# Kernel tuning notes

Measured on AMD Instinct MI355X. Metric: run time of the kernel, lower is better.

The kernel has to match this reference:

```python
import jax, jax.numpy as jnp
import numpy as np

K = 16
D = 1024
B = 65536

# Row-major off-diagonal index order matching the torch double loop (i, j, i != j)
_ii, _jj = np.nonzero(~np.eye(K, dtype=bool))  # each (K*(K-1),), row-major
OFF_I = jnp.asarray(_ii)
OFF_J = jnp.asarray(_jj)
DIAG = jnp.arange(K)


def setup_inputs() -> dict:
    key = jax.random.key(0)
    k1, k2, k3, k4, k5 = jax.random.split(key, 5)
    scale_d = 1.0 / np.sqrt(D)
    return {
        "x": jax.random.normal(k1, (B, D), dtype=jnp.float32),
        "Wd": jax.random.normal(k2, (K, D), dtype=jnp.float32) * scale_d,
        "bd": jax.random.normal(k3, (K,), dtype=jnp.float32) * 0.1,
        "Wo": jax.random.normal(k4, (K * (K - 1), D), dtype=jnp.float32) * scale_d,
        "bo": jax.random.normal(k5, (K * (K - 1),), dtype=jnp.float32) * 0.1 - 3.0,
    }


def reference(x, Wd, bd, Wo, bo):
    # Diagonal gates: (B, K)
    c_diag = jax.nn.sigmoid(jnp.einsum("bd,kd->bk", x, Wd) + bd)
    # Off-diagonal values: (B, K*(K-1)), non-positive
    off_vals = -jax.nn.softplus(jnp.einsum("bd,kd->bk", x, Wo) + bo)
    C = jnp.zeros((x.shape[0], K, K), dtype=x.dtype)
    C = C.at[:, OFF_I, OFF_J].set(off_vals)
    C = C.at[:, DIAG, DIAG].set(c_diag)
    return C
```

## Files before the change

kernel.cpp:

```cpp
#include <hip/hip_runtime.h>
#include <hip/hip_bf16.h>
#include <stdint.h>


typedef __bf16 bf16x8 __attribute__((ext_vector_type(8)));
typedef float f32x4 __attribute__((ext_vector_type(4)));

#define THREADS 512
#define BM 128
#define KSTEPS 32
#define WIMG 16384
#define WBYTES (WIMG * KSTEPS)

#define ASLOT 16384
#define BBASE 49152
#define BSLOT 16384
#define SMEM_SZ 81920

__device__ __forceinline__ unsigned bf_rtne(unsigned u) {
  return (u + 0x7fffu + ((u >> 16) & 1u)) >> 16;
}
__device__ __forceinline__ unsigned pack2(float lo, float hi) {
  return bf_rtne(__float_as_uint(lo)) | (bf_rtne(__float_as_uint(hi)) << 16);
}
__device__ __forceinline__ bf16x8 packfrag(const f32x4& a, const f32x4& b) {
  bf16x8 r;
  r[0] = (__bf16)a[0]; r[1] = (__bf16)a[1]; r[2] = (__bf16)a[2]; r[3] = (__bf16)a[3];
  r[4] = (__bf16)b[0]; r[5] = (__bf16)b[1]; r[6] = (__bf16)b[2]; r[7] = (__bf16)b[3];
  return r;
}
__device__ __forceinline__ void gload_lds16(const void* g, void* l) {
  __builtin_amdgcn_global_load_lds(
      (const __attribute__((address_space(1))) unsigned int*)g,
      (__attribute__((address_space(3))) unsigned int*)l, 16, 0, 0);
}

__global__ void prep_kernel(const float* __restrict__ Wd, const float* __restrict__ bd,
                            const float* __restrict__ Wo, const float* __restrict__ bo,
                            char* __restrict__ wbuf, float* __restrict__ bias) {
  const int c = blockIdx.x;
  const int t = threadIdx.x;
  const int i = c >> 4, j = c & 15;
  const float* src;
  float b;
  if (i == j) { src = Wd + i * 1024; b = bd[i]; }
  else { int r = i * 15 + (j < i ? j : j - 1); src = Wo + r * 1024; b = bo[r]; }
  if (t == 0) bias[c] = b;
  const int kk = t * 4;
  const int img = kk >> 5, k5 = kk & 31;
  float4 v = *reinterpret_cast<const float4*>(src + kk);
  uint2 h;
  h.x = pack2(v.x, v.y);
  h.y = pack2(v.z, v.w);
  const unsigned off = (unsigned)((c * 64 + k5 * 2) ^ (((c >> 1) & 3) << 4));
  *reinterpret_cast<uint2*>(wbuf + img * WIMG + off) = h;
}

__global__ __launch_bounds__(THREADS, 4) void cap_main(
    const float* __restrict__ x, const char* __restrict__ wbuf,
    const float* __restrict__ bias, float* __restrict__ out) {
  __shared__ char smem[SMEM_SZ];

  const int tid = threadIdx.x;
  const int wid = tid >> 6;
  const int lane = tid & 63;
  const int l15 = lane & 15;
  const int l4 = lane >> 4;
  const int wm = wid >> 2;
  const int wn = wid & 3;

  const size_t blkRow = (size_t)blockIdx.x * BM;

  const unsigned acol = (unsigned)(((tid & 7) * 16) ^ (((tid >> 3) & 7) << 4));
  const char* asrc[2];
  unsigned adst[2];
#pragma unroll
  for (int i = 0; i < 2; ++i) {
    const int row = i * 64 + (tid >> 3);
    asrc[i] = (const char*)(x + (blkRow + (size_t)row) * 1024) + acol;
    adst[i] = (unsigned)(i * 8192 + tid * 16);
  }

  const unsigned swA = (unsigned)((l15 & 7) << 4);
  const unsigned bbase = (unsigned)(wn * 4096 + l15 * 64 +
                                    ((l4 * 16) ^ (((l15 >> 1) & 3) << 4)));

  f32x4 acc[4][4];
#pragma unroll
  for (int m = 0; m < 4; ++m)
#pragma unroll
    for (int n = 0; n < 4; ++n) acc[m][n] = (f32x4){0.f, 0.f, 0.f, 0.f};

#define STAGE_A(CH, SL)                                                        \
  {                                                                            \
    _Pragma("unroll") for (int i = 0; i < 2; ++i)                              \
        gload_lds16(asrc[i] + (CH) * 128, smem + (SL) + adst[i]);              \
  }
#define STAGE_B(CH, SL)                                                        \
  {                                                                            \
    const char* wsp = wbuf + (CH) * WIMG;                                      \
    _Pragma("unroll") for (int i = 0; i < 2; ++i)                              \
        gload_lds16(wsp + i * 8192 + tid * 16,                                 \
                    smem + BBASE + (SL) + i * 8192 + tid * 16);                \
  }

  STAGE_A(0, 0);
  STAGE_B(0, 0);
  STAGE_A(1, ASLOT);
  asm volatile("s_waitcnt vmcnt(2)\n\ts_barrier" ::: "memory");

  unsigned aR = 0;
  unsigned aI = 2 * ASLOT;
  unsigned bR = 0;

  for (int t = 0; t < KSTEPS; ++t) {
    const int tb = (t + 1 < KSTEPS) ? t + 1 : KSTEPS - 1;
    STAGE_B(tb, bR ^ BSLOT);
    const int ta = (t + 2 < KSTEPS) ? t + 2 : KSTEPS - 1;
    STAGE_A(ta, aI);

    const char* Ac = smem + aR;
    const char* Bc = smem + BBASE + bR;
    bf16x8 af[4], bfr[4];
#pragma unroll
    for (int m = 0; m < 4; ++m) {
      const unsigned rb = (unsigned)((wm * 64 + m * 16 + l15) * 128);
      f32x4 u0 = *reinterpret_cast<const f32x4*>(Ac + rb + ((l4 * 32) ^ swA));
      f32x4 u1 = *reinterpret_cast<const f32x4*>(Ac + rb + ((l4 * 32 + 16) ^ swA));
      af[m] = packfrag(u0, u1);
    }
#pragma unroll
    for (int n = 0; n < 4; ++n)
      bfr[n] = *reinterpret_cast<const bf16x8*>(Bc + bbase + n * 1024);

#pragma unroll
    for (int m = 0; m < 4; ++m)
#pragma unroll
      for (int n = 0; n < 4; ++n)
        acc[m][n] = __builtin_amdgcn_mfma_f32_16x16x32_bf16(af[m], bfr[n], acc[m][n], 0, 0, 0);

    asm volatile("s_waitcnt vmcnt(2)" ::: "memory");
    asm volatile("s_waitcnt lgkmcnt(0)" ::: "memory");
    __builtin_amdgcn_s_barrier();

    aR = (aR == 2 * ASLOT) ? 0u : aR + ASLOT;
    aI = (aI == 2 * ASLOT) ? 0u : aI + ASLOT;
    bR ^= BSLOT;
  }
#undef STAGE_A
#undef STAGE_B

  asm volatile("s_waitcnt vmcnt(0)" ::: "memory");
  __syncthreads();

  float bs[4];
#pragma unroll
  for (int n = 0; n < 4; ++n) bs[n] = bias[wn * 64 + n * 16 + l15];

  const int rr2 = tid >> 5;
  const int co = (tid & 31) * 8;
  const char* rdp = smem + rr2 * 1040 + co * 4;

#pragma unroll
  for (int p = 0; p < 8; ++p) {
    if ((wid >> 2) == (p >> 2)) {
      const int m = p & 3;
#pragma unroll
      for (int n = 0; n < 4; ++n) {
        const int col = wn * 64 + n * 16 + l15;
        const bool diag = (col % 17) == 0;
#pragma unroll
        for (int j2 = 0; j2 < 4; ++j2) {
          const int rr = l4 * 4 + j2;
          float v = acc[m][n][j2] + bs[n];
          float e = __expf(-fabsf(v));
          float sig = (v >= 0.f) ? 1.f / (1.f + e) : e / (1.f + e);
          float sp = fmaxf(v, 0.f) + __logf(1.f + e);
          *reinterpret_cast<float*>(smem + rr * 1040 + col * 4) = diag ? sig : -sp;
        }
      }
    }
    __syncthreads();
    float4 o0 = *reinterpret_cast<const float4*>(rdp);
    float4 o1 = *reinterpret_cast<const float4*>(rdp + 16);
    float* orow = out + (blkRow + (size_t)(p * 16 + rr2)) * 256 + co;
    *reinterpret_cast<float4*>(orow) = o0;
    *reinterpret_cast<float4*>(orow + 4) = o1;
    __syncthreads();
  }
}

extern "C" void kernel_launch(void* const* d_in, const int* in_sizes, int n_in,
                              void* d_out, int out_size, void* d_ws, size_t ws_size,
                              hipStream_t stream) {
  const float* x = (const float*)d_in[0];
  const float* Wd = (const float*)d_in[1];
  const float* bd = (const float*)d_in[2];
  const float* Wo = (const float*)d_in[3];
  const float* bo = (const float*)d_in[4];
  float* out = (float*)d_out;
  char* wbuf = (char*)d_ws;
  float* bias = (float*)(wbuf + WBYTES);

  prep_kernel<<<dim3(256), dim3(256), 0, stream>>>(Wd, bd, Wo, bo, wbuf, bias);
  cap_main<<<dim3(512), dim3(THREADS), 0, stream>>>(x, wbuf, bias, out);
}
```

Measured before the change: 100.2 us.

## Double K-chunk size to 64 and switch to two-stage double-buffered pipeline

Each loop iteration now processes a 64-wide K chunk as two MFMA substeps, halving the number of barrier-synchronised iterations. The A ring buffer drops from triple to double buffering, and every iteration waits for all outstanding loads (vmcnt(0)). Shared memory grows to 128 KB per block and the occupancy hint of 4 in launch_bounds is removed, so fewer blocks fit per CU. The weight image and swizzle layout are rewritten to match the 128-byte-per-row chunks. Less prefetch depth may expose load latency in exchange for fewer barriers.

```diff
diff --git a/kernel.cpp b/kernel.cpp
--- a/kernel.cpp
+++ b/kernel.cpp
@@ -8,14 +8,14 @@
 
 #define THREADS 512
 #define BM 128
-#define KSTEPS 32
-#define WIMG 16384
-#define WBYTES (WIMG * KSTEPS)
-
-#define ASLOT 16384
-#define BBASE 49152
-#define BSLOT 16384
-#define SMEM_SZ 81920
+#define NCHUNK 16
+#define CIMG 32768
+#define WBYTES (CIMG * NCHUNK)
+
+#define ASLOT 32768
+#define BBASE 65536
+#define BSLOT 32768
+#define SMEM_SZ 131072
 
 __device__ __forceinline__ unsigned bf_rtne(unsigned u) {
   return (u + 0x7fffu + ((u >> 16) & 1u)) >> 16;
@@ -47,16 +47,16 @@
   else { int r = i * 15 + (j < i ? j : j - 1); src = Wo + r * 1024; b = bo[r]; }
   if (t == 0) bias[c] = b;
   const int kk = t * 4;
-  const int img = kk >> 5, k5 = kk & 31;
+  const int chunk = kk >> 6, k6 = kk & 63;
   float4 v = *reinterpret_cast<const float4*>(src + kk);
   uint2 h;
   h.x = pack2(v.x, v.y);
   h.y = pack2(v.z, v.w);
-  const unsigned off = (unsigned)((c * 64 + k5 * 2) ^ (((c >> 1) & 3) << 4));
-  *reinterpret_cast<uint2*>(wbuf + img * WIMG + off) = h;
-}
-
-__global__ __launch_bounds__(THREADS, 4) void cap_main(
+  const unsigned off = (unsigned)(c * 128 + ((k6 * 2) ^ ((c & 7) << 4)));
+  *reinterpret_cast<uint2*>(wbuf + chunk * CIMG + off) = h;
+}
+
+__global__ __launch_bounds__(THREADS) void cap_main(
     const float* __restrict__ x, const char* __restrict__ wbuf,
     const float* __restrict__ bias, float* __restrict__ out) {
   __shared__ char smem[SMEM_SZ];
@@ -71,19 +71,19 @@
 
   const size_t blkRow = (size_t)blockIdx.x * BM;
 
-  const unsigned acol = (unsigned)(((tid & 7) * 16) ^ (((tid >> 3) & 7) << 4));
-  const char* asrc[2];
-  unsigned adst[2];
-#pragma unroll
-  for (int i = 0; i < 2; ++i) {
-    const int row = i * 64 + (tid >> 3);
+  const unsigned acol = (unsigned)(((tid & 15) * 16) ^ ((((tid >> 4) & 15)) << 4));
+  const char* asrc[4];
+  unsigned adst[4];
+#pragma unroll
+  for (int i = 0; i < 4; ++i) {
+    const int row = i * 32 + (tid >> 4);
     asrc[i] = (const char*)(x + (blkRow + (size_t)row) * 1024) + acol;
     adst[i] = (unsigned)(i * 8192 + tid * 16);
   }
 
-  const unsigned swA = (unsigned)((l15 & 7) << 4);
-  const unsigned bbase = (unsigned)(wn * 4096 + l15 * 64 +
-                                    ((l4 * 16) ^ (((l15 >> 1) & 3) << 4)));
+  const unsigned swA = (unsigned)(l15 << 4);
+  const unsigned swB = (unsigned)((l15 & 7) << 4);
+  const unsigned bcol = (unsigned)((wn * 64 + l15) * 128);
 
   f32x4 acc[4][4];
 #pragma unroll
@@ -93,64 +93,62 @@
 
 #define STAGE_A(CH, SL)                                                        \
   {                                                                            \
-    _Pragma("unroll") for (int i = 0; i < 2; ++i)                              \
-        gload_lds16(asrc[i] + (CH) * 128, smem + (SL) + adst[i]);              \
+    _Pragma("unroll") for (int i = 0; i < 4; ++i)                              \
+        gload_lds16(asrc[i] + (CH) * 256, smem + (SL) + adst[i]);              \
   }
 #define STAGE_B(CH, SL)                                                        \
   {                                                                            \
-    const char* wsp = wbuf + (CH) * WIMG;                                      \
-    _Pragma("unroll") for (int i = 0; i < 2; ++i)                              \
+    const char* wsp = wbuf + (CH) * CIMG;                                      \
+    _Pragma("unroll") for (int i = 0; i < 4; ++i)                              \
         gload_lds16(wsp + i * 8192 + tid * 16,                                 \
                     smem + BBASE + (SL) + i * 8192 + tid * 16);                \
   }
 
   STAGE_A(0, 0);
   STAGE_B(0, 0);
-  STAGE_A(1, ASLOT);
-  asm volatile("s_waitcnt vmcnt(2)\n\ts_barrier" ::: "memory");
-
-  unsigned aR = 0;
-  unsigned aI = 2 * ASLOT;
-  unsigned bR = 0;
-
-  for (int t = 0; t < KSTEPS; ++t) {
-    const int tb = (t + 1 < KSTEPS) ? t + 1 : KSTEPS - 1;
-    STAGE_B(tb, bR ^ BSLOT);
-    const int ta = (t + 2 < KSTEPS) ? t + 2 : KSTEPS - 1;
-    STAGE_A(ta, aI);
-
-    const char* Ac = smem + aR;
-    const char* Bc = smem + BBASE + bR;
-    bf16x8 af[4], bfr[4];
-#pragma unroll
-    for (int m = 0; m < 4; ++m) {
-      const unsigned rb = (unsigned)((wm * 64 + m * 16 + l15) * 128);
-      f32x4 u0 = *reinterpret_cast<const f32x4*>(Ac + rb + ((l4 * 32) ^ swA));
-      f32x4 u1 = *reinterpret_cast<const f32x4*>(Ac + rb + ((l4 * 32 + 16) ^ swA));
-      af[m] = packfrag(u0, u1);
+  asm volatile("s_waitcnt vmcnt(0)" ::: "memory");
+  __builtin_amdgcn_s_barrier();
+
+  for (int t = 0; t < NCHUNK; ++t) {
+    const unsigned sc = (unsigned)(t & 1);
+    const unsigned sn = sc ^ 1u;
+
+    const int tn = (t + 1 < NCHUNK) ? t + 1 : NCHUNK - 1;
+    STAGE_B(tn, sn * BSLOT);
+    STAGE_A(tn, sn * ASLOT);
+
+    const char* Ac = smem + sc * ASLOT;
+    const char* Bc = smem + BBASE + sc * BSLOT;
+
+#pragma unroll
+    for (int ks = 0; ks < 2; ++ks) {
+      bf16x8 af[4], bfr[4];
+#pragma unroll
+      for (int m = 0; m < 4; ++m) {
+        const unsigned rb = (unsigned)((wm * 64 + m * 16 + l15) * 256);
+        f32x4 u0 = *reinterpret_cast<const f32x4*>(
+            Ac + rb + ((ks * 128 + l4 * 32) ^ swA));
+        f32x4 u1 = *reinterpret_cast<const f32x4*>(
+            Ac + rb + ((ks * 128 + l4 * 32 + 16) ^ swA));
+        af[m] = packfrag(u0, u1);
+      }
+#pragma unroll
+      for (int n = 0; n < 4; ++n)
+        bfr[n] = *reinterpret_cast<const bf16x8*>(
+            Bc + bcol + n * 2048 + ((ks * 64 + l4 * 16) ^ swB));
+#pragma unroll
+      for (int m = 0; m < 4; ++m)
+#pragma unroll
+        for (int n = 0; n < 4; ++n)
+          acc[m][n] = __builtin_amdgcn_mfma_f32_16x16x32_bf16(af[m], bfr[n], acc[m][n], 0, 0, 0);
     }
-#pragma unroll
-    for (int n = 0; n < 4; ++n)
-      bfr[n] = *reinterpret_cast<const bf16x8*>(Bc + bbase + n * 1024);
-
-#pragma unroll
-    for (int m = 0; m < 4; ++m)
-#pragma unroll
-      for (int n = 0; n < 4; ++n)
-        acc[m][n] = __builtin_amdgcn_mfma_f32_16x16x32_bf16(af[m], bfr[n], acc[m][n], 0, 0, 0);
-
-    asm volatile("s_waitcnt vmcnt(2)" ::: "memory");
-    asm volatile("s_waitcnt lgkmcnt(0)" ::: "memory");
+
+    asm volatile("s_waitcnt vmcnt(0) lgkmcnt(0)" ::: "memory");
     __builtin_amdgcn_s_barrier();
-
-    aR = (aR == 2 * ASLOT) ? 0u : aR + ASLOT;
-    aI = (aI == 2 * ASLOT) ? 0u : aI + ASLOT;
-    bR ^= BSLOT;
   }
 #undef STAGE_A
 #undef STAGE_B
 
-  asm volatile("s_waitcnt vmcnt(0)" ::: "memory");
   __syncthreads();
 
   float bs[4];
```

Result: slower. 111.6 us (+11.4%).
